# Kernel optimization log

Measured on AMD Instinct MI355X. Metric: run time of the kernel, lower is better.

The kernel has to match this reference:

```python
import jax, jax.numpy as jnp
import numpy as np

N_EMBD = 1024
N_HEAD = 16
HEAD_DIM = N_EMBD // N_HEAD  # 64; scale = sqrt(64) = 8


def setup_inputs() -> dict:
    key = jax.random.key(0)
    k0, k1, k2, k3, k4 = jax.random.split(key, 5)
    B, T = 4, 2048
    x = jax.random.normal(k0, (B, T, N_EMBD), dtype=jnp.float32)
    # torch Linear weights are (out,in); we store (in,out) so y = x @ W + b
    W_attn = jax.random.normal(k1, (N_EMBD, 3 * N_EMBD), dtype=jnp.float32) * 0.02
    b_attn = jax.random.normal(k2, (3 * N_EMBD,), dtype=jnp.float32) * 0.02
    W_proj = jax.random.normal(k3, (N_EMBD, N_EMBD), dtype=jnp.float32) * 0.02
    b_proj = jax.random.normal(k4, (N_EMBD,), dtype=jnp.float32) * 0.02
    return {"x": x, "W_attn": W_attn, "b_attn": b_attn,
            "W_proj": W_proj, "b_proj": b_proj}


def reference(x, W_attn, b_attn, W_proj, b_proj):
    B, T, D = x.shape
    scale = 1.0 / np.float32(np.sqrt(HEAD_DIM))
    qkv = x @ W_attn + b_attn                      # [B,T,3D]
    q, k, v = jnp.split(qkv, 3, axis=-1)           # each [B,T,D]
    att = jnp.einsum('bid,bjd->bij', q, k) * scale # [B,T,T]
    causal = jnp.tril(jnp.ones((T, T), dtype=bool))
    att = jnp.where(causal[None, :, :], att, jnp.float32(-jnp.inf))
    att = jax.nn.softmax(att, axis=-1)
    y = jnp.einsum('bij,bjd->bid', att, v)         # [B,T,D]
    return y @ W_proj + b_proj
```

## Files before the change

kernel.cpp:

```cpp
#include <hip/hip_runtime.h>

typedef __attribute__((ext_vector_type(8))) short short8;
typedef __attribute__((ext_vector_type(4))) float f32x4;
typedef __attribute__((ext_vector_type(4))) unsigned short ushort4v;

__device__ __forceinline__ unsigned short f2bf(float f) {
  unsigned int u = __float_as_uint(f);
  u += 0x7fffu + ((u >> 16) & 1u);
  return (unsigned short)(u >> 16);
}
__device__ __forceinline__ float bf2f(unsigned short h) {
  return __uint_as_float(((unsigned int)h) << 16);
}

__device__ __forceinline__ void gload16(const unsigned short* g, unsigned short* l) {
  __builtin_amdgcn_global_load_lds(
      (const __attribute__((address_space(1))) unsigned int*)g,
      (__attribute__((address_space(3))) unsigned int*)l,
      16, 0, 0);
}

__device__ __forceinline__ void bar() {
  asm volatile("" ::: "memory");
  __builtin_amdgcn_s_barrier();
  asm volatile("" ::: "memory");
}

__global__ __launch_bounds__(256) void conv_x_kernel(const float* __restrict__ x,
                                                     unsigned short* __restrict__ xb) {
  int i = blockIdx.x * 256 + threadIdx.x;
  f32x4 v = ((const f32x4*)x)[i];
  ushort4v o;
  o[0] = f2bf(v[0]); o[1] = f2bf(v[1]); o[2] = f2bf(v[2]); o[3] = f2bf(v[3]);
  ((ushort4v*)xb)[i] = o;
}

__global__ __launch_bounds__(256) void transpose_w_kernel(const float* __restrict__ W,
                                                          unsigned short* __restrict__ Wt,
                                                          int K, int N) {
  __shared__ float tile[32][33];
  int n0 = blockIdx.x * 32, k0 = blockIdx.y * 32;
  int tx = threadIdx.x, ty = threadIdx.y;
#pragma unroll
  for (int j = 0; j < 32; j += 8)
    tile[ty + j][tx] = W[(size_t)(k0 + ty + j) * N + n0 + tx];
  __syncthreads();
#pragma unroll
  for (int j = 0; j < 32; j += 8)
    Wt[(size_t)(n0 + ty + j) * K + k0 + tx] = f2bf(tile[tx][ty + j]);
}

__global__ __launch_bounds__(256) void transpose_v_kernel(const unsigned short* __restrict__ qkv,
                                                          unsigned short* __restrict__ vt) {
  __shared__ unsigned short tile[32][33];
  int b = blockIdx.z;
  int key0 = blockIdx.x * 32, d0 = blockIdx.y * 32;
  int tx = threadIdx.x, ty = threadIdx.y;
#pragma unroll
  for (int j = 0; j < 32; j += 8)
    tile[ty + j][tx] = qkv[(size_t)(b * 2048 + key0 + ty + j) * 3072 + 2048 + d0 + tx];
  __syncthreads();
#pragma unroll
  for (int j = 0; j < 32; j += 8)
    vt[(size_t)(b * 1024 + d0 + ty + j) * 2048 + key0 + tx] = tile[tx][ty + j];
}

__global__ __launch_bounds__(256) void softmax_kernel(unsigned short* __restrict__ S) {
  int row = blockIdx.x * 4 + (threadIdx.x >> 6);
  int l = threadIdx.x & 63;
  unsigned short* p = S + (size_t)row * 2048;
  float v[32];
#pragma unroll
  for (int i = 0; i < 4; i++) {
    short8 raw = *(const short8*)&p[(i * 64 + l) * 8];
#pragma unroll
    for (int j = 0; j < 8; j++) v[i * 8 + j] = bf2f((unsigned short)raw[j]);
  }
  float mx = -3e38f;
#pragma unroll
  for (int i = 0; i < 32; i++) mx = fmaxf(mx, v[i]);
#pragma unroll
  for (int off = 1; off < 64; off <<= 1) mx = fmaxf(mx, __shfl_xor(mx, off));
  float s = 0.f;
#pragma unroll
  for (int i = 0; i < 32; i++) { v[i] = exp2f((v[i] - mx) * 1.44269504f); s += v[i]; }
#pragma unroll
  for (int off = 1; off < 64; off <<= 1) s += __shfl_xor(s, off);
  float inv = 1.f / s;
#pragma unroll
  for (int i = 0; i < 4; i++) {
    short8 o;
#pragma unroll
    for (int j = 0; j < 8; j++) o[j] = (short)f2bf(v[i * 8 + j] * inv);
    *(short8*)&p[(i * 64 + l) * 8] = o;
  }
}

template <int OUTBF>
__global__ __launch_bounds__(256) void gemm128_kernel(
    const unsigned short* __restrict__ A, int lda, long long saz,
    const unsigned short* __restrict__ Bt, int ldb, long long sbz,
    void* __restrict__ Cv, int ldc, long long scz,
    const float* __restrict__ bias, int K, float scale, int causal) {
  __shared__ __align__(16) unsigned short lds[4][8192];

  const int m0 = blockIdx.y * 128, n0 = blockIdx.x * 128;
  const int z = blockIdx.z;
  A += (size_t)z * saz;
  Bt += (size_t)z * sbz;

  const int t = threadIdx.x;
  const int lane = t & 63, wid = t >> 6;
  const int g = lane >> 4, q = lane & 15;
  const int wm = wid >> 1, wn = wid & 1;

  int NT = K >> 5;
  if (causal == 1) { if (n0 >= m0 + 128) NT = 0; }
  else if (causal == 2) { NT = min(K, m0 + 128) >> 5; }

  f32x4 acc[4][4] = {};

  if (NT > 0) {
    const int csrc = ((t & 3) ^ ((t >> 2) & 3) ^ ((t >> 4) & 3)) * 8;
    const unsigned short* aS = A + (size_t)(m0 + (t >> 2)) * lda + csrc;
    const unsigned short* bS = Bt + (size_t)(n0 + (t >> 2)) * ldb + csrc;

    auto stage = [&](int tt) {
      unsigned short* d = &lds[tt & 3][wid * 512];
      const unsigned short* sa = aS + tt * 32;
      const unsigned short* sb = bS + tt * 32;
      gload16(sa, d);
      gload16(sa + (size_t)64 * lda, d + 2048);
      gload16(sb, d + 4096);
      gload16(sb + (size_t)64 * ldb, d + 6144);
    };

    const int chunk = (g ^ (q & 3) ^ ((q >> 2) & 3)) * 8;
    const int aOff = (wm * 64 + q) * 32 + chunk;
    const int bOff = 4096 + (wn * 64 + q) * 32 + chunk;

    stage(0);
    if (NT > 1) stage(1);

    for (int tt = 0; tt < NT; ++tt) {
      if (tt + 2 < NT) {
        stage(tt + 2);
        asm volatile("s_waitcnt vmcnt(8)" ::: "memory");
      } else if (tt + 1 < NT) {
        asm volatile("s_waitcnt vmcnt(4)" ::: "memory");
      } else {
        asm volatile("s_waitcnt vmcnt(0)" ::: "memory");
      }
      bar();

      const unsigned short* buf = lds[tt & 3];
      short8 af[4], bb[4];
#pragma unroll
      for (int m = 0; m < 4; m++) af[m] = *(const short8*)&buf[aOff + m * 512];
#pragma unroll
      for (int n = 0; n < 4; n++) bb[n] = *(const short8*)&buf[bOff + n * 512];
#pragma unroll
      for (int m = 0; m < 4; m++)
#pragma unroll
        for (int n = 0; n < 4; n++)
          acc[m][n] = __builtin_amdgcn_mfma_f32_16x16x32_bf16(af[m], bb[n], acc[m][n], 0, 0, 0);
    }
  }

#pragma unroll
  for (int n = 0; n < 4; n++) {
    int colg = n0 + wn * 64 + n * 16 + q;
    float bv = bias ? bias[colg] : 0.f;
#pragma unroll
    for (int m = 0; m < 4; m++) {
      int rowb = m0 + wm * 64 + m * 16 + g * 4;
#pragma unroll
      for (int r = 0; r < 4; r++) {
        float val = acc[m][n][r] * scale + bv;
        if (causal == 1 && colg > rowb + r) val = -1e30f;
        if (OUTBF) {
          ((unsigned short*)Cv)[(size_t)z * scz + (size_t)(rowb + r) * ldc + colg] = f2bf(val);
        } else {
          ((float*)Cv)[(size_t)z * scz + (size_t)(rowb + r) * ldc + colg] = val;
        }
      }
    }
  }
}

extern "C" void kernel_launch(void* const* d_in, const int* in_sizes, int n_in,
                              void* d_out, int out_size, void* d_ws, size_t ws_size,
                              hipStream_t stream) {
  const float* x  = (const float*)d_in[0];
  const float* Wa = (const float*)d_in[1];
  const float* ba = (const float*)d_in[2];
  const float* Wp = (const float*)d_in[3];
  const float* bp = (const float*)d_in[4];
  float* out = (float*)d_out;

  char* ws = (char*)d_ws;
  unsigned short* qkv = (unsigned short*)(ws);
  unsigned short* xb  = (unsigned short*)(ws + 50331648);
  unsigned short* vt  = (unsigned short*)(ws + 50331648);
  unsigned short* wta = (unsigned short*)(ws + 67108864);
  unsigned short* S   = (unsigned short*)(ws + 73400320);
  unsigned short* y   = (unsigned short*)(ws + 106954752);
  unsigned short* wtp = (unsigned short*)(ws + 123731968);

  conv_x_kernel<<<8192, 256, 0, stream>>>(x, xb);
  transpose_w_kernel<<<dim3(96, 32), dim3(32, 8), 0, stream>>>(Wa, wta, 1024, 3072);
  transpose_w_kernel<<<dim3(32, 32), dim3(32, 8), 0, stream>>>(Wp, wtp, 1024, 1024);

  gemm128_kernel<1><<<dim3(24, 64, 1), 256, 0, stream>>>(
      xb, 1024, 0, wta, 1024, 0, qkv, 3072, 0, ba, 1024, 1.0f, 0);

  gemm128_kernel<1><<<dim3(16, 16, 4), 256, 0, stream>>>(
      qkv, 3072, 2048LL * 3072, qkv + 1024, 3072, 2048LL * 3072,
      S, 2048, 2048LL * 2048, nullptr, 1024, 0.125f, 1);

  softmax_kernel<<<2048, 256, 0, stream>>>(S);

  transpose_v_kernel<<<dim3(64, 32, 4), dim3(32, 8), 0, stream>>>(qkv, vt);

  gemm128_kernel<1><<<dim3(8, 16, 4), 256, 0, stream>>>(
      S, 2048, 2048LL * 2048, vt, 2048, 1024LL * 2048,
      y, 1024, 2048LL * 1024, nullptr, 2048, 1.0f, 2);

  gemm128_kernel<0><<<dim3(8, 64, 1), 256, 0, stream>>>(
      y, 1024, 0, wtp, 1024, 0, out, 1024, 0, bp, 1024, 1.0f, 0);
}
```

Measured before the change: 219.6 us.

## Use K=64 tiles with double-buffered LDS and inline-asm reads in GEMM

The GEMM main loop now loads K=64 tiles (instead of 32) into two LDS buffers rather than four, using a new XOR swizzle. Fragments are read with inline ds_read_b128 at constant offsets, and the MFMA block is raised in priority with s_setprio. The loop is unrolled by two so buffer addresses are compile-time constants. The aim is fewer barriers and loop iterations per unit of K and better MFMA issue density. In exchange, prefetch depth drops from two tiles ahead to one, with a full vmcnt(0) wait before each barrier, which may expose more global-load latency.

```diff
diff --git a/kernel.cpp b/kernel.cpp
--- a/kernel.cpp
+++ b/kernel.cpp
@@ -3,6 +3,9 @@
 typedef __attribute__((ext_vector_type(8))) short short8;
 typedef __attribute__((ext_vector_type(4))) float f32x4;
 typedef __attribute__((ext_vector_type(4))) unsigned short ushort4v;
+
+struct DB0 { static constexpr int value = 0; };
+struct DB1 { static constexpr int value = 1; };
 
 __device__ __forceinline__ unsigned short f2bf(float f) {
   unsigned int u = __float_as_uint(f);
@@ -18,6 +21,13 @@
       (const __attribute__((address_space(1))) unsigned int*)g,
       (__attribute__((address_space(3))) unsigned int*)l,
       16, 0, 0);
+}
+
+template <int OFF>
+__device__ __forceinline__ short8 dsr(unsigned a) {
+  short8 r;
+  asm volatile("ds_read_b128 %0, %1 offset:%2" : "=v"(r) : "v"(a), "n"(OFF));
+  return r;
 }
 
 __device__ __forceinline__ void bar() {
@@ -102,7 +112,7 @@
     const unsigned short* __restrict__ Bt, int ldb, long long sbz,
     void* __restrict__ Cv, int ldc, long long scz,
     const float* __restrict__ bias, int K, float scale, int causal) {
-  __shared__ __align__(16) unsigned short lds[4][8192];
+  __shared__ __align__(16) unsigned short lds[2][16384];
 
   const int m0 = blockIdx.y * 128, n0 = blockIdx.x * 128;
   const int z = blockIdx.z;
@@ -114,57 +124,79 @@
   const int g = lane >> 4, q = lane & 15;
   const int wm = wid >> 1, wn = wid & 1;
 
-  int NT = K >> 5;
+  int NT = K >> 6;
   if (causal == 1) { if (n0 >= m0 + 128) NT = 0; }
-  else if (causal == 2) { NT = min(K, m0 + 128) >> 5; }
+  else if (causal == 2) { NT = min(K, m0 + 128) >> 6; }
 
   f32x4 acc[4][4] = {};
 
   if (NT > 0) {
-    const int csrc = ((t & 3) ^ ((t >> 2) & 3) ^ ((t >> 4) & 3)) * 8;
-    const unsigned short* aS = A + (size_t)(m0 + (t >> 2)) * lda + csrc;
-    const unsigned short* bS = Bt + (size_t)(n0 + (t >> 2)) * ldb + csrc;
+    const int scol = ((t & 7) * 8) ^ ((t & 32) >> 1);
+    const unsigned short* aS = A + (size_t)(m0 + (t >> 3)) * lda + scol;
+    const unsigned short* bS = Bt + (size_t)(n0 + (t >> 3)) * ldb + scol;
 
     auto stage = [&](int tt) {
-      unsigned short* d = &lds[tt & 3][wid * 512];
-      const unsigned short* sa = aS + tt * 32;
-      const unsigned short* sb = bS + tt * 32;
+      unsigned short* d = &lds[tt & 1][wid * 512];
+      const unsigned short* sa = aS + (size_t)tt * 64;
+      const unsigned short* sb = bS + (size_t)tt * 64;
       gload16(sa, d);
-      gload16(sa + (size_t)64 * lda, d + 2048);
-      gload16(sb, d + 4096);
-      gload16(sb + (size_t)64 * ldb, d + 6144);
+      gload16(sa + (size_t)32 * lda, d + 2048);
+      gload16(sa + (size_t)64 * lda, d + 4096);
+      gload16(sa + (size_t)96 * lda, d + 6144);
+      gload16(sb, d + 8192);
+      gload16(sb + (size_t)32 * ldb, d + 10240);
+      gload16(sb + (size_t)64 * ldb, d + 12288);
+      gload16(sb + (size_t)96 * ldb, d + 14336);
     };
 
-    const int chunk = (g ^ (q & 3) ^ ((q >> 2) & 3)) * 8;
-    const int aOff = (wm * 64 + q) * 32 + chunk;
-    const int bOff = 4096 + (wn * 64 + q) * 32 + chunk;
+    const unsigned base =
+        (unsigned)(unsigned long long)(__attribute__((address_space(3))) unsigned short*)&lds[0][0];
+    const int colA = (g * 16) ^ ((q & 4) << 3);
+    const unsigned aaB = base + (unsigned)((wm * 64 + q) * 128 + colA);
+    const unsigned bbB = base + 16384u + (unsigned)((wn * 64 + q) * 128 + colA);
 
     stage(0);
-    if (NT > 1) stage(1);
-
-    for (int tt = 0; tt < NT; ++tt) {
-      if (tt + 2 < NT) {
-        stage(tt + 2);
-        asm volatile("s_waitcnt vmcnt(8)" ::: "memory");
-      } else if (tt + 1 < NT) {
-        asm volatile("s_waitcnt vmcnt(4)" ::: "memory");
-      } else {
-        asm volatile("s_waitcnt vmcnt(0)" ::: "memory");
+    asm volatile("s_waitcnt vmcnt(0)" ::: "memory");
+    bar();
+
+    auto body = [&](auto dbc, int tt) {
+      constexpr int DB = decltype(dbc)::value;
+      const unsigned aa = aaB + DB * 32768u;
+      const unsigned bb = bbB + DB * 32768u;
+      if (tt + 1 < NT) stage(tt + 1);
+      short8 aq[4][2], bq[4][2];
+#pragma unroll
+      for (int m = 0; m < 4; m++) {
+        aq[m][0] = dsr<0>(aa + m * 2048u);
+        aq[m][1] = dsr<64>(aa + m * 2048u);
       }
+#pragma unroll
+      for (int n = 0; n < 4; n++) {
+        bq[n][0] = dsr<0>(bb + n * 2048u);
+        bq[n][1] = dsr<64>(bb + n * 2048u);
+      }
+      asm volatile("s_waitcnt lgkmcnt(0)" ::: "memory");
+      __builtin_amdgcn_sched_barrier(0);
+      __builtin_amdgcn_s_setprio(1);
+#pragma unroll
+      for (int ks = 0; ks < 2; ks++)
+#pragma unroll
+        for (int m = 0; m < 4; m++)
+#pragma unroll
+          for (int n = 0; n < 4; n++)
+            acc[m][n] = __builtin_amdgcn_mfma_f32_16x16x32_bf16(aq[m][ks], bq[n][ks], acc[m][n], 0, 0, 0);
+      __builtin_amdgcn_s_setprio(0);
+      __builtin_amdgcn_sched_barrier(0);
+      asm volatile("s_waitcnt vmcnt(0)" ::: "memory");
       bar();
-
-      const unsigned short* buf = lds[tt & 3];
-      short8 af[4], bb[4];
-#pragma unroll
-      for (int m = 0; m < 4; m++) af[m] = *(const short8*)&buf[aOff + m * 512];
-#pragma unroll
-      for (int n = 0; n < 4; n++) bb[n] = *(const short8*)&buf[bOff + n * 512];
-#pragma unroll
-      for (int m = 0; m < 4; m++)
-#pragma unroll
-        for (int n = 0; n < 4; n++)
-          acc[m][n] = __builtin_amdgcn_mfma_f32_16x16x32_bf16(af[m], bb[n], acc[m][n], 0, 0, 0);
+    };
+
+    int tt = 0;
+    for (; tt + 2 <= NT; tt += 2) {
+      body(DB0{}, tt);
+      body(DB1{}, tt + 1);
     }
+    if (tt < NT) body(DB0{}, tt);
   }
 
 #pragma unroll
```

Measured after the change: 204.6 us. 1.07x faster.
